# Kernel tuning notes

Measured on AMD Instinct MI355X. Metric: run time of the kernel, lower is better.

Reference implementation:

```python
import jax, jax.numpy as jnp
import numpy as np

SEQ = 8          # sequence_size
C = 128          # in_channels / factor (hidden + input channels)
BN_EPS = 1e-5


def setup_inputs() -> dict:
    key = jax.random.key(0)
    k1, k2 = jax.random.split(key)
    x = jax.random.normal(k1, (32, C, 64, 64), dtype=jnp.float32)          # (B*T, C, H, W)
    w_conv = jax.random.normal(k2, (4 * C, 2 * C, 3, 3), dtype=jnp.float32) * 0.05  # OIHW
    b_conv = jnp.zeros((4 * C,), dtype=jnp.float32)
    gamma = jnp.ones((C,), dtype=jnp.float32)
    beta = jnp.zeros((C,), dtype=jnp.float32)
    run_mean = jnp.zeros((C,), dtype=jnp.float32)
    run_var = jnp.ones((C,), dtype=jnp.float32)
    return {"x": x, "w_conv": w_conv, "b_conv": b_conv, "gamma": gamma,
            "beta": beta, "run_mean": run_mean, "run_var": run_var}


def _convlstm_scan(x_seq, w_conv, b_conv):
    # x_seq: (B, T, C, H, W); zero initial (h, c) states (reset path)
    B, T, Cc, H, W = x_seq.shape
    h0 = jnp.zeros((B, Cc, H, W), x_seq.dtype)
    c0 = jnp.zeros((B, Cc, H, W), x_seq.dtype)

    def step(carry, x_t):
        h, c = carry
        z = jax.lax.conv_general_dilated(
            jnp.concatenate([x_t, h], axis=1), w_conv,
            window_strides=(1, 1), padding='SAME',
            dimension_numbers=('NCHW', 'OIHW', 'NCHW'))
        z = z + b_conv[None, :, None, None]
        i, f, o, g = jnp.split(z, 4, axis=1)
        c_next = jax.nn.sigmoid(f) * c + jax.nn.sigmoid(i) * jnp.tanh(g)
        h_next = jax.nn.sigmoid(o) * jnp.tanh(c_next)
        return (h_next, c_next), h_next

    _, hs = jax.lax.scan(step, (h0, c0), jnp.swapaxes(x_seq, 0, 1))  # hs: (T, B, C, H, W)
    return jnp.swapaxes(hs, 0, 1)  # (B, T, C, H, W)


def reference(x, w_conv, b_conv, gamma, beta, run_mean, run_var):
    BT, Cc, H, W = x.shape
    x_seq = x.reshape(BT // SEQ, SEQ, Cc, H, W)
    hs = _convlstm_scan(x_seq, w_conv, b_conv)           # (B, T, C, H, W)
    out = hs.reshape(-1, Cc, H, W)                        # (B*T, C, H, W)
    # BatchNorm2d (eval mode: running stats) + ReLU
    inv = jax.lax.rsqrt(run_var + BN_EPS)
    out = (out - run_mean[None, :, None, None]) * (inv * gamma)[None, :, None, None] \
          + beta[None, :, None, None]
    return jax.nn.relu(out)
```

## Files before the change

kernel.cpp:

```cpp
#include <hip/hip_runtime.h>
#include <hip/hip_bf16.h>
#include <math.h>

typedef __attribute__((ext_vector_type(8))) short bf16x8;
typedef __attribute__((ext_vector_type(4))) float f32x4;

#define FRAME_PAD (66*66*128)

#define GLOAD_LDS16(g, l) \
    __builtin_amdgcn_global_load_lds((const __attribute__((address_space(1))) void*)(g), \
                                     (__attribute__((address_space(3))) void*)(l), 16, 0, 0)

#define WAITV8    asm volatile("s_waitcnt vmcnt(8)" ::: "memory")
#define WAITV0    asm volatile("s_waitcnt vmcnt(0)" ::: "memory")
#define WAITLGKM0 asm volatile("s_waitcnt lgkmcnt(0)" ::: "memory")
#define SBAR      __builtin_amdgcn_s_barrier()

__device__ __forceinline__ float sigmoidf_(float x) { return 1.0f / (1.0f + __expf(-x)); }
__device__ __forceinline__ float tanhf_(float x) {
    x = fminf(fmaxf(x, -15.0f), 15.0f);
    float e = __expf(2.0f * x);
    return (e - 1.0f) / (e + 1.0f);
}
__device__ __forceinline__ float b2f_(short u) {
    unsigned int v = ((unsigned int)(unsigned short)u) << 16;
    return __builtin_bit_cast(float, v);
}
__device__ __forceinline__ short f2b_(float f) {
    __hip_bfloat16 hb = __float2bfloat16(f);
    return *reinterpret_cast<short*>(&hb);
}

__global__ void wt_kernel(const float* __restrict__ w, __hip_bfloat16* __restrict__ wt)
{
    int idx = blockIdx.x * 256 + threadIdx.x;
    if (idx >= 9 * 512 * 256) return;
    int ic  = idx & 255;
    int n   = (idx >> 8) & 511;
    int tap = idx >> 17;
    int c = n >> 2, g = n & 3;
    int oc = g * 128 + c;
    wt[idx] = __float2bfloat16(w[((size_t)oc * 256 + (size_t)ic) * 9 + tap]);
}

__global__ void border_kernel(__hip_bfloat16* __restrict__ x_pad,
                              __hip_bfloat16* __restrict__ h_pad)
{
    const int fr = blockIdx.x;
    __hip_bfloat16* base = (fr < 32) ? x_pad + (size_t)fr * FRAME_PAD
                                     : h_pad + (size_t)(fr - 32) * FRAME_PAD;
    bf16x8 z = {};
    for (int u = threadIdx.x; u < 2112; u += 256) {
        int half = (u >= 1056) ? 1 : 0;
        int v = u - half * 1056;
        *(bf16x8*)(base + (size_t)(half * 65 * 66) * 128 + (size_t)v * 8) = z;
    }
    for (int u = threadIdx.x; u < 2048; u += 256) {
        int yy = 1 + (u >> 5);
        int r = u & 31;
        int side = r >> 4, c16 = r & 15;
        *(bf16x8*)(base + (size_t)(yy * 66 + side * 65) * 128 + (size_t)c16 * 8) = z;
    }
}

__global__ void xpose_kernel(const float* __restrict__ x, __hip_bfloat16* __restrict__ x_pad)
{
    __shared__ float tile[64][129];
    const int f = blockIdx.x >> 6;
    const int y = blockIdx.x & 63;
    const int tid = threadIdx.x;
    const float* src = x + (size_t)f * 524288 + (size_t)y * 64;
    #pragma unroll
    for (int it = 0; it < 8; ++it) {
        int c  = it * 16 + (tid >> 4);
        int xq = tid & 15;
        float4 v = *(const float4*)(src + (size_t)c * 4096 + xq * 4);
        tile[xq * 4 + 0][c] = v.x;
        tile[xq * 4 + 1][c] = v.y;
        tile[xq * 4 + 2][c] = v.z;
        tile[xq * 4 + 3][c] = v.w;
    }
    __syncthreads();
    __hip_bfloat16* dst = x_pad + (size_t)f * FRAME_PAD + (size_t)((y + 1) * 66 + 1) * 128;
    const int g = tid & 15;
    #pragma unroll
    for (int it = 0; it < 4; ++it) {
        int xr = it * 16 + (tid >> 4);
        bf16x8 o;
        #pragma unroll
        for (int e = 0; e < 8; ++e) o[e] = f2b_(tile[xr][g * 8 + e]);
        *(bf16x8*)(dst + (size_t)xr * 128 + g * 8) = o;
    }
}

template<bool T0>
__global__ __launch_bounds__(256, 2)
void conv_gemm(const __hip_bfloat16* __restrict__ x_pad,
               const __hip_bfloat16* __restrict__ h_pad,
               const __hip_bfloat16* __restrict__ wt,
               const float* __restrict__ bias,
               const float* __restrict__ gamma, const float* __restrict__ beta,
               const float* __restrict__ rmean, const float* __restrict__ rvar,
               float* __restrict__ c_state, float* __restrict__ out, int t)
{
    __shared__ alignas(16) __hip_bfloat16 S_s[2][128 * 64];
    __shared__ alignas(16) __hip_bfloat16 W_s[2][128 * 64];
    const int tid  = threadIdx.x;
    const int wv   = tid >> 6;
    const int lane = tid & 63;
    const int KT   = T0 ? 18 : 36;

    const int F    = blockIdx.x;
    const int tile = (F >> 3) + (F & 7) * 64;
    const int n0   = (tile & 3) * 128;
    const int mblk = tile >> 2;
    const int b    = mblk >> 5;
    const int y0   = (mblk & 31) * 2;
    const int m0   = mblk * 128;

    const __hip_bfloat16* xf = x_pad + (size_t)(b * 8 + t) * FRAME_PAD;
    const __hip_bfloat16* hf = T0 ? xf
                                  : h_pad + (size_t)(b * 8 + t - 1) * FRAME_PAD;

    int aOff[4], bOff[4];
    #pragma unroll
    for (int j = 0; j < 4; ++j) {
        int sid = j * 256 + tid;
        int row = sid >> 3;
        int q   = (sid & 7) ^ (row & 7);
        aOff[j] = ((y0 + (row >> 6)) * 66 + (row & 63)) * 128 + q * 8;
        bOff[j] = (n0 + row) * 256 + q * 8;
    }

    auto STAGE = [&](__hip_bfloat16* Sl, __hip_bfloat16* Wl, int kt) {
        int tap, icq;
        const __hip_bfloat16* sb;
        if constexpr (T0) { tap = kt >> 1; icq = (kt & 1) * 64; sb = xf + icq; }
        else { tap = kt >> 2; icq = (kt & 3) * 64;
               sb = (icq < 128) ? (xf + icq) : (hf + (icq - 128)); }
        const int dy = tap / 3, dx = tap % 3;
        const __hip_bfloat16* a = sb + (dy * 66 + dx) * 128;
        #pragma unroll
        for (int j = 0; j < 4; ++j)
            GLOAD_LDS16(a + aOff[j], Sl + (size_t)(j * 256 + tid) * 8);
        const __hip_bfloat16* bsrc = wt + tap * 131072 + icq;
        #pragma unroll
        for (int j = 0; j < 4; ++j)
            GLOAD_LDS16(bsrc + bOff[j], Wl + (size_t)(j * 256 + tid) * 8);
    };

    const int wm = wv >> 1, wn = wv & 1;
    const int fr = lane & 15, fq = lane >> 4;
    const int slot = (fq ^ (fr & 7)) * 8;
    const int sOff0 = (wm * 64 + fr) * 64 + slot, sOff1 = sOff0 ^ 32;
    const int wOff0 = (wn * 64 + fr) * 64 + slot, wOff1 = wOff0 ^ 32;

    f32x4 acc[4][4] = {};

    auto ITER = [&](__hip_bfloat16* Sb, __hip_bfloat16* Wb, int kt) {
        if (kt < KT - 1) { WAITV8; } else { WAITV0; }
        SBAR;
        bf16x8 w0[4], w1[4], s0[4], s1[4];
        #pragma unroll
        for (int ri = 0; ri < 4; ++ri) {
            w0[ri] = *(const bf16x8*)(Wb + wOff0 + ri * 1024);
            w1[ri] = *(const bf16x8*)(Wb + wOff1 + ri * 1024);
        }
        #pragma unroll
        for (int ci = 0; ci < 4; ++ci) {
            s0[ci] = *(const bf16x8*)(Sb + sOff0 + ci * 1024);
            s1[ci] = *(const bf16x8*)(Sb + sOff1 + ci * 1024);
        }
        __builtin_amdgcn_s_setprio(1);
        #pragma unroll
        for (int ri = 0; ri < 4; ++ri)
            #pragma unroll
            for (int ci = 0; ci < 4; ++ci)
                acc[ri][ci] = __builtin_amdgcn_mfma_f32_16x16x32_bf16(w0[ri], s0[ci], acc[ri][ci], 0, 0, 0);
        __builtin_amdgcn_s_setprio(0);
        WAITLGKM0;
        __builtin_amdgcn_sched_barrier(0);
        SBAR;
        if (kt < KT - 2) STAGE(Sb, Wb, kt + 2);
        __builtin_amdgcn_s_setprio(1);
        #pragma unroll
        for (int ri = 0; ri < 4; ++ri)
            #pragma unroll
            for (int ci = 0; ci < 4; ++ci)
                acc[ri][ci] = __builtin_amdgcn_mfma_f32_16x16x32_bf16(w1[ri], s1[ci], acc[ri][ci], 0, 0, 0);
        __builtin_amdgcn_s_setprio(0);
    };

    STAGE(S_s[0], W_s[0], 0);
    STAGE(S_s[1], W_s[1], 1);
    #pragma unroll 1
    for (int kt = 0; kt < KT; kt += 2) {
        ITER(S_s[0], W_s[0], kt);
        ITER(S_s[1], W_s[1], kt + 1);
    }

    const int c0    = (n0 >> 2) + wn * 16;
    const int mcol0 = m0 + wm * 64 + fr;
    __hip_bfloat16* hout = (__hip_bfloat16*)h_pad + (size_t)(b * 8 + t) * FRAME_PAD;
    float* oframe = out + (size_t)(b * 8 + t) * 524288;
    #pragma unroll
    for (int ri = 0; ri < 4; ++ri) {
        const int c = c0 + ri * 4 + fq;
        const float bi  = bias[c];
        const float bfv = bias[128 + c];
        const float bo  = bias[256 + c];
        const float bg  = bias[384 + c];
        const float scv = gamma[c] * rsqrtf(rvar[c] + 1e-5f);
        const float shv = beta[c] - rmean[c] * scv;
        float* csrow = c_state + (size_t)c * 16384;
        #pragma unroll
        for (int ci = 0; ci < 4; ++ci) {
            const int m = mcol0 + ci * 16;
            const int s = m & 4095;
            const float cold = T0 ? 0.0f : csrow[m];
            const float zi = acc[ri][ci][0] + bi;
            const float zf = acc[ri][ci][1] + bfv;
            const float zo = acc[ri][ci][2] + bo;
            const float zg = acc[ri][ci][3] + bg;
            const float cn = sigmoidf_(zf) * cold + sigmoidf_(zi) * tanhf_(zg);
            const float h  = sigmoidf_(zo) * tanhf_(cn);
            csrow[m] = cn;
            hout[(size_t)(((s >> 6) + 1) * 66 + (s & 63) + 1) * 128 + c] = __float2bfloat16(h);
            oframe[(size_t)c * 4096 + s] = fmaxf(h * scv + shv, 0.0f);
        }
    }
}

extern "C" void kernel_launch(void* const* d_in, const int* in_sizes, int n_in,
                              void* d_out, int out_size, void* d_ws, size_t ws_size,
                              hipStream_t stream)
{
    const float* x      = (const float*)d_in[0];
    const float* w_conv = (const float*)d_in[1];
    const float* b_conv = (const float*)d_in[2];
    const float* gamma  = (const float*)d_in[3];
    const float* beta   = (const float*)d_in[4];
    const float* rmean  = (const float*)d_in[5];
    const float* rvar   = (const float*)d_in[6];
    float* out = (float*)d_out;

    if (ws_size < 82116608u) return;

    char* ws = (char*)d_ws;
    __hip_bfloat16* Wt    = (__hip_bfloat16*)(ws);
    __hip_bfloat16* x_pad = (__hip_bfloat16*)(ws + 2359296);
    __hip_bfloat16* h_pad = (__hip_bfloat16*)(ws + 38043648);
    float* c_state        = (float*)(ws + 73728000);

    wt_kernel<<<4608, 256, 0, stream>>>(w_conv, Wt);
    xpose_kernel<<<2048, 256, 0, stream>>>(x, x_pad);
    border_kernel<<<64, 256, 0, stream>>>(x_pad, h_pad);

    conv_gemm<true><<<512, 256, 0, stream>>>(x_pad, h_pad, Wt, b_conv,
                                             gamma, beta, rmean, rvar, c_state, out, 0);
    for (int t = 1; t < 8; ++t)
        conv_gemm<false><<<512, 256, 0, stream>>>(x_pad, h_pad, Wt, b_conv,
                                                  gamma, beta, rmean, rvar, c_state, out, t);
}
```

Measured before the change: 352.0 us.

## Load conv weights directly into registers instead of staging through LDS

```diff
diff --git a/kernel.cpp b/kernel.cpp
--- a/kernel.cpp
+++ b/kernel.cpp
@@ -11,7 +11,7 @@
     __builtin_amdgcn_global_load_lds((const __attribute__((address_space(1))) void*)(g), \
                                      (__attribute__((address_space(3))) void*)(l), 16, 0, 0)
 
-#define WAITV8    asm volatile("s_waitcnt vmcnt(8)" ::: "memory")
+#define WAITV4    asm volatile("s_waitcnt vmcnt(4)" ::: "memory")
 #define WAITV0    asm volatile("s_waitcnt vmcnt(0)" ::: "memory")
 #define WAITLGKM0 asm volatile("s_waitcnt lgkmcnt(0)" ::: "memory")
 #define SBAR      __builtin_amdgcn_s_barrier()
@@ -104,7 +104,6 @@
                float* __restrict__ c_state, float* __restrict__ out, int t)
 {
     __shared__ alignas(16) __hip_bfloat16 S_s[2][128 * 64];
-    __shared__ alignas(16) __hip_bfloat16 W_s[2][128 * 64];
     const int tid  = threadIdx.x;
     const int wv   = tid >> 6;
     const int lane = tid & 63;
@@ -122,17 +121,16 @@
     const __hip_bfloat16* hf = T0 ? xf
                                   : h_pad + (size_t)(b * 8 + t - 1) * FRAME_PAD;
 
-    int aOff[4], bOff[4];
+    int aOff[4];
     #pragma unroll
     for (int j = 0; j < 4; ++j) {
         int sid = j * 256 + tid;
         int row = sid >> 3;
         int q   = (sid & 7) ^ (row & 7);
         aOff[j] = ((y0 + (row >> 6)) * 66 + (row & 63)) * 128 + q * 8;
-        bOff[j] = (n0 + row) * 256 + q * 8;
-    }
-
-    auto STAGE = [&](__hip_bfloat16* Sl, __hip_bfloat16* Wl, int kt) {
+    }
+
+    auto STAGE_A = [&](__hip_bfloat16* Sl, int kt) {
         int tap, icq;
         const __hip_bfloat16* sb;
         if constexpr (T0) { tap = kt >> 1; icq = (kt & 1) * 64; sb = xf + icq; }
@@ -143,29 +141,35 @@
         #pragma unroll
         for (int j = 0; j < 4; ++j)
             GLOAD_LDS16(a + aOff[j], Sl + (size_t)(j * 256 + tid) * 8);
-        const __hip_bfloat16* bsrc = wt + tap * 131072 + icq;
-        #pragma unroll
-        for (int j = 0; j < 4; ++j)
-            GLOAD_LDS16(bsrc + bOff[j], Wl + (size_t)(j * 256 + tid) * 8);
     };
 
     const int wm = wv >> 1, wn = wv & 1;
     const int fr = lane & 15, fq = lane >> 4;
+
+    const __hip_bfloat16* wlane = wt + (size_t)(n0 + wn * 64 + fr) * 256 + fq * 8;
+    auto LOADW = [&](bf16x8* wreg, int kt) {
+        int tap, icq;
+        if constexpr (T0) { tap = kt >> 1; icq = (kt & 1) * 64; }
+        else { tap = kt >> 2; icq = (kt & 3) * 64; }
+        const __hip_bfloat16* p = wlane + (size_t)tap * 131072 + icq;
+        #pragma unroll
+        for (int ri = 0; ri < 4; ++ri) {
+            wreg[ri]     = *(const bf16x8*)(p + ri * 4096);
+            wreg[4 + ri] = *(const bf16x8*)(p + ri * 4096 + 32);
+        }
+    };
+
     const int slot = (fq ^ (fr & 7)) * 8;
     const int sOff0 = (wm * 64 + fr) * 64 + slot, sOff1 = sOff0 ^ 32;
-    const int wOff0 = (wn * 64 + fr) * 64 + slot, wOff1 = wOff0 ^ 32;
 
     f32x4 acc[4][4] = {};
-
-    auto ITER = [&](__hip_bfloat16* Sb, __hip_bfloat16* Wb, int kt) {
-        if (kt < KT - 1) { WAITV8; } else { WAITV0; }
+    bf16x8 wA[8], wB[8];
+
+    auto ITER = [&](__hip_bfloat16* Sb, bf16x8* wuse, bf16x8* wload, int kt) {
+        if (kt < KT - 1) { WAITV4; } else { WAITV0; }
         SBAR;
-        bf16x8 w0[4], w1[4], s0[4], s1[4];
-        #pragma unroll
-        for (int ri = 0; ri < 4; ++ri) {
-            w0[ri] = *(const bf16x8*)(Wb + wOff0 + ri * 1024);
-            w1[ri] = *(const bf16x8*)(Wb + wOff1 + ri * 1024);
-        }
+        if (kt < KT - 1) LOADW(wload, kt + 1);
+        bf16x8 s0[4], s1[4];
         #pragma unroll
         for (int ci = 0; ci < 4; ++ci) {
             s0[ci] = *(const bf16x8*)(Sb + sOff0 + ci * 1024);
@@ -176,27 +180,28 @@
         for (int ri = 0; ri < 4; ++ri)
             #pragma unroll
             for (int ci = 0; ci < 4; ++ci)
-                acc[ri][ci] = __builtin_amdgcn_mfma_f32_16x16x32_bf16(w0[ri], s0[ci], acc[ri][ci], 0, 0, 0);
+                acc[ri][ci] = __builtin_amdgcn_mfma_f32_16x16x32_bf16(wuse[ri], s0[ci], acc[ri][ci], 0, 0, 0);
         __builtin_amdgcn_s_setprio(0);
         WAITLGKM0;
         __builtin_amdgcn_sched_barrier(0);
         SBAR;
-        if (kt < KT - 2) STAGE(Sb, Wb, kt + 2);
+        if (kt < KT - 2) STAGE_A(Sb, kt + 2);
         __builtin_amdgcn_s_setprio(1);
         #pragma unroll
         for (int ri = 0; ri < 4; ++ri)
             #pragma unroll
             for (int ci = 0; ci < 4; ++ci)
-                acc[ri][ci] = __builtin_amdgcn_mfma_f32_16x16x32_bf16(w1[ri], s1[ci], acc[ri][ci], 0, 0, 0);
+                acc[ri][ci] = __builtin_amdgcn_mfma_f32_16x16x32_bf16(wuse[4 + ri], s1[ci], acc[ri][ci], 0, 0, 0);
         __builtin_amdgcn_s_setprio(0);
     };
 
-    STAGE(S_s[0], W_s[0], 0);
-    STAGE(S_s[1], W_s[1], 1);
+    STAGE_A(S_s[0], 0);
+    LOADW(wA, 0);
+    STAGE_A(S_s[1], 1);
     #pragma unroll 1
     for (int kt = 0; kt < KT; kt += 2) {
-        ITER(S_s[0], W_s[0], kt);
-        ITER(S_s[1], W_s[1], kt + 1);
+        ITER(S_s[0], wA, wB, kt);
+        ITER(S_s[1], wB, wA, kt + 1);
     }
 
     const int c0    = (n0 >> 2) + wn * 16;
```

Result: slower. 648.2 us (+84.2%).
